# Performance work log

Hardware: AMD Instinct MI355X
Metric: run time of the kernel (lower is better)

The kernel has to match this reference:

```python
import jax, jax.numpy as jnp
import numpy as np

N, E, IN, H, OUT = 50000, 600000, 256, 128, 40
EPS, GAMMA = 0.1, 0.1  # PyG AntiSymmetricConv defaults


def _build_norm(edge_index, n):
    # GCNConv normalization with added self loops: D^-1/2 (A+I) D^-1/2
    loops = jnp.arange(n, dtype=edge_index.dtype)
    src = jnp.concatenate([edge_index[0], loops])
    dst = jnp.concatenate([edge_index[1], loops])
    deg = jax.ops.segment_sum(jnp.ones(src.shape[0], dtype=jnp.float32), dst, num_segments=n)
    dinv = jnp.where(deg > 0, jax.lax.rsqrt(jnp.maximum(deg, 1e-12)), 0.0)
    return src, dst, dinv[src] * dinv[dst]


def _gcn(x, w, src, dst, norm, n):
    # GCNConv(bias=False): scatter normalized messages to target nodes
    m = (x @ w)[src] * norm[:, None]          # [E+N, d]
    return jax.ops.segment_sum(m, dst, num_segments=n)


def _antisym_conv(x, W, gcn_w, bias, src, dst, norm, num_iters):
    d = W.shape[0]
    aW = W - W.T - GAMMA * jnp.eye(d, dtype=W.dtype)  # antisymmetric weight
    n = x.shape[0]

    def step(h, _):
        upd = jnp.tanh(h @ aW.T + _gcn(h, gcn_w, src, dst, norm, n) + bias)
        return h + EPS * upd, None

    x, _ = jax.lax.scan(step, x, None, length=num_iters)
    return x


def setup_inputs() -> dict:
    key = jax.random.key(0)
    ks = jax.random.split(key, 16)
    s = lambda fan: 1.0 / np.sqrt(fan)
    return {
        "x": jax.random.normal(ks[0], (N, IN), dtype=jnp.float32),
        "edge_index": jax.random.randint(ks[1], (2, E), 0, N, dtype=jnp.int64),
        "w_hid": jax.random.normal(ks[2], (H, IN), dtype=jnp.float32) * s(IN),
        "b_hid": jax.random.normal(ks[3], (H,), dtype=jnp.float32) * s(IN),
        "W_a1": jax.random.normal(ks[4], (H, H), dtype=jnp.float32) * s(H),
        "gcn_w1": jax.random.normal(ks[5], (H, H), dtype=jnp.float32) * s(H),
        "b_a1": jax.random.normal(ks[6], (H,), dtype=jnp.float32) * s(H),
        "w_hid2": jax.random.normal(ks[7], (H // 2, H), dtype=jnp.float32) * s(H),
        "b_hid2": jax.random.normal(ks[8], (H // 2,), dtype=jnp.float32) * s(H),
        "W_a2": jax.random.normal(ks[9], (H // 2, H // 2), dtype=jnp.float32) * s(H // 2),
        "gcn_w2": jax.random.normal(ks[10], (H // 2, H // 2), dtype=jnp.float32) * s(H // 2),
        "b_a2": jax.random.normal(ks[11], (H // 2,), dtype=jnp.float32) * s(H // 2),
        "w_fc": jax.random.normal(ks[12], (OUT, H // 2), dtype=jnp.float32) * s(H // 2),
        "b_fc": jax.random.normal(ks[13], (OUT,), dtype=jnp.float32) * s(H // 2),
    }


def reference(x, edge_index, w_hid, b_hid, W_a1, gcn_w1, b_a1,
              w_hid2, b_hid2, W_a2, gcn_w2, b_a2, w_fc, b_fc):
    n = x.shape[0]
    src, dst, norm = _build_norm(edge_index, n)
    h = jax.nn.leaky_relu(x @ w_hid.T + b_hid)          # dropout is no-op in eval
    h = _antisym_conv(h, W_a1, gcn_w1, b_a1, src, dst, norm, num_iters=3)
    h = jax.nn.leaky_relu(h)
    h = jax.nn.leaky_relu(h @ w_hid2.T + b_hid2)
    h = _antisym_conv(h, W_a2, gcn_w2, b_a2, src, dst, norm, num_iters=1)
    out = h @ w_fc.T + b_fc
    return jax.nn.log_softmax(out, axis=1)
```

## Files before the change

kernel.cpp:

```cpp
#include <hip/hip_runtime.h>
#include <hip/hip_bf16.h>
#include <math.h>

typedef unsigned short u16;
typedef unsigned int   u32;
using short8  = __attribute__((ext_vector_type(8))) short;
using f32x4   = __attribute__((ext_vector_type(4))) float;

static constexpr int NNODE = 50000;
static constexpr int NEDGE = 600000;
static constexpr float EPSC   = 0.1f;
static constexpr float GAMMAC = 0.1f;

static constexpr int NTILE = (NNODE + 63) / 64;
static constexpr int GH    = 128;
static constexpr int NRNG  = 12500;
static constexpr int NWORD = NRNG / 2;
static constexpr int NPASS = 4;

static constexpr long long O_DINV   = 0;
static constexpr long long O_DEGI   = 50000;
static constexpr long long O_ROWPTR = 100000;
static constexpr long long O_GCUR   = 150004;
static constexpr long long O_ECSR   = 200260;
static constexpr long long O_WHB    = 1400260;
static constexpr long long O_G1TB   = O_WHB  + 16384;
static constexpr long long O_AW1B   = O_G1TB + 8192;
static constexpr long long O_W2B    = O_AW1B + 8192;
static constexpr long long O_AW2B   = O_W2B  + 4096;
static constexpr long long O_G2TB   = O_AW2B + 2048;
static constexpr long long O_WFCB   = O_G2TB + 2048;
static constexpr long long O_AGGB   = 3450004;
static constexpr long long O_HB0    = O_AGGB + 3200000;
static constexpr long long O_HB1    = O_HB0  + 3200000;
static constexpr long long O_S0     = O_HB1  + 3200000;
static constexpr long long O_S1     = O_S0   + 1600000;
static constexpr long long O_PART   = O_S1   + 1600000;
static constexpr long long O_BASE   = O_PART + 3200000;

__device__ __forceinline__ float bf2f(u16 u) {
    return __uint_as_float(((unsigned)u) << 16);
}
__device__ __forceinline__ u16 f2bf(float f) {
    unsigned u = __float_as_uint(f);
    return (u16)((u + 0x7FFFu + ((u >> 16) & 1u)) >> 16);
}
__device__ __forceinline__ float ftanh(float x) {
    float x2 = fminf(fmaxf(2.f * x, -30.f), 30.f);
    float e = __expf(x2);
    return (e - 1.f) * __builtin_amdgcn_rcpf(e + 1.f);
}
__device__ __forceinline__ u16 pk_fp8(float a, float b) {
    int pk = __builtin_amdgcn_cvt_pk_fp8_f32(a, b, 0, false);
    return (u16)(pk & 0xffff);
}
__device__ __forceinline__ void acc_fp8x4(float* a, u32 v, float w) {
    a[0] += __builtin_amdgcn_cvt_f32_fp8(v, 0) * w;
    a[1] += __builtin_amdgcn_cvt_f32_fp8(v, 1) * w;
    a[2] += __builtin_amdgcn_cvt_f32_fp8(v, 2) * w;
    a[3] += __builtin_amdgcn_cvt_f32_fp8(v, 3) * w;
}

__global__ __launch_bounds__(256) void prep_kernel(
    const float* __restrict__ w_hid, const float* __restrict__ W_a1,
    const float* __restrict__ gcn1,  const float* __restrict__ w2,
    const float* __restrict__ W_a2,  const float* __restrict__ gcn2,
    const float* __restrict__ wfc,   float* __restrict__ ws)
{
    int j = blockIdx.x * 256 + threadIdx.x;
    if (j < 32768) { ((u16*)(ws+O_WHB))[j] = f2bf(w_hid[j]); return; } j -= 32768;
    if (j < 16384) { int r=j>>7, c=j&127; ((u16*)(ws+O_G1TB))[j] = f2bf(gcn1[c*128+r]); return; } j -= 16384;
    if (j < 16384) { int r=j>>7, c=j&127;
                     ((u16*)(ws+O_AW1B))[j] = f2bf(W_a1[r*128+c] - W_a1[c*128+r] - (r==c?GAMMAC:0.f));
                     return; } j -= 16384;
    if (j < 8192)  { ((u16*)(ws+O_W2B))[j] = f2bf(w2[j]); return; } j -= 8192;
    if (j < 4096)  { int r=j>>6, c=j&63;
                     ((u16*)(ws+O_AW2B))[j] = f2bf(W_a2[r*64+c] - W_a2[c*64+r] - (r==c?GAMMAC:0.f));
                     return; } j -= 4096;
    if (j < 4096)  { int r=j>>6, c=j&63; ((u16*)(ws+O_G2TB))[j] = f2bf(gcn2[c*64+r]); return; } j -= 4096;
    if (j < 2560)  { ((u16*)(ws+O_WFCB))[j] = f2bf(wfc[j]); return; } j -= 2560;
    if (j == 0)    { ((int*)(ws+O_GCUR))[0] = 0; }
}

__global__ __launch_bounds__(256) void alloc_kernel(
    const u16* __restrict__ part, float* __restrict__ dinv,
    int* __restrict__ degi, int* __restrict__ rowptr,
    u16* __restrict__ base16, int* __restrict__ gcur)
{
    int i = blockIdx.x * 256 + threadIdx.x;
    int lane = threadIdx.x & 63;
    bool ok = i < NNODE;
    int deg = 0;
    if (ok) {
        int run = 0;
        #pragma unroll 4
        for (int g = 0; g < GH; ++g) {
            base16[(long long)g * NNODE + i] = (u16)run;
            run += part[(long long)g * NNODE + i];
        }
        deg = run;
        degi[i] = deg;
        dinv[i] = rsqrtf(1.0f + (float)deg);
    }
    int run = deg;
    #pragma unroll
    for (int off = 1; off < 64; off <<= 1) {
        int v = __shfl_up(run, off);
        if (lane >= off) run += v;
    }
    int tot = __shfl(run, 63);
    int basep = 0;
    if (lane == 63) basep = atomicAdd(gcur, tot);
    basep = __shfl(basep, 63);
    if (ok) rowptr[i] = basep + run - deg;
}

__global__ __launch_bounds__(256) void fill_kernel(
    const int* __restrict__ ei, const float* __restrict__ dinv,
    const int* __restrict__ rowptr, const u16* __restrict__ base16,
    int2* __restrict__ ecsr)
{
    __shared__ u32 cur[NWORD];
    const int g    = blockIdx.x >> 2;
    const int pass = blockIdx.x & 3;
    const long long e0 = (long long)g * NEDGE / GH;
    const long long e1 = (long long)(g + 1) * NEDGE / GH;
    const u16* bb = base16 + (long long)g * NNODE;
    const int nbase = pass * NRNG;
    for (int wi = threadIdx.x; wi < NWORD; wi += 256) cur[wi] = 0;
    __syncthreads();
    for (long long e = e0 + threadIdx.x; e < e1; e += 256) {
        int d = ei[NEDGE + e];
        int r = d - nbase;
        if ((unsigned)r < (unsigned)NRNG) {
            int s = ei[e];
            u32 old = atomicAdd(&cur[r >> 1], 1u << ((r & 1) * 16));
            int rank = (int)((old >> ((r & 1) * 16)) & 0xffffu);
            int slot = rowptr[d] + (int)bb[d] + rank;
            int2 v;
            v.x = s;
            v.y = __float_as_int(dinv[s]);
            ecsr[slot] = v;
        }
    }
}

template<int KS, int NT, int AF32, int LOADACT, int EPI>
__global__ __launch_bounds__(256, 4) void mgemm(
    const void* __restrict__ Araw,
    const u16* __restrict__ Bt,
    const float* __restrict__ bias,
    float* __restrict__ outF,
    u16* __restrict__ outB,
    u16* __restrict__ outB8,
    int M, int Nn, int ldc,
    const int* __restrict__ ei,
    u16* __restrict__ partial)
{
    constexpr int K    = KS * 32;
    constexpr int KCHU = (K > 128) ? 128 : K;
    constexpr int KC   = KCHU / 32;
    constexpr int NCH  = K / KCHU;
    constexpr int P    = KCHU + 8;
    constexpr int ROWS = NT * 16;
    constexpr int CW   = NT * 16 + 1;
    constexpr int BSZ  = ROWS * P * 2;
    constexpr int ASZ  = 64 * CW * 4;
    constexpr int SMEM = BSZ > ASZ ? BSZ : ASZ;
    __shared__ __align__(16) char smem[SMEM];

    if (ei && blockIdx.x >= NTILE) {
        int g = blockIdx.x - NTILE;
        u32* hist = (u32*)smem;
        const long long e0 = (long long)g * NEDGE / GH;
        const long long e1 = (long long)(g + 1) * NEDGE / GH;
        u16* part = partial + (long long)g * NNODE;
        for (int pass = 0; pass < NPASS; ++pass) {
            const int nbase = pass * NRNG;
            for (int wi = threadIdx.x; wi < NWORD; wi += 256) hist[wi] = 0;
            __syncthreads();
            for (long long e = e0 + threadIdx.x; e < e1; e += 256) {
                int d = ei[NEDGE + e];
                int r = d - nbase;
                if ((unsigned)r < (unsigned)NRNG)
                    atomicAdd(&hist[r >> 1], 1u << ((r & 1) * 16));
            }
            __syncthreads();
            for (int wi = threadIdx.x; wi < NWORD; wi += 256)
                *(u32*)&part[nbase + wi * 2] = hist[wi];
            __syncthreads();
        }
        return;
    }

    u16*   bl   = (u16*)smem;
    float* accL = (float*)smem;

    const int wave = threadIdx.x >> 6;
    const int lane = threadIdx.x & 63;
    const int m = lane & 15, q = lane >> 4;
    const int rowbase = blockIdx.x * 64 + wave * 16;
    const int row = rowbase + m;
    const bool rok = row < M;
    const short8 z8 = {0,0,0,0,0,0,0,0};

    short8 af[KS];
    if (AF32) {
        const float* apf = (const float*)Araw + (long long)row * K;
        #pragma unroll
        for (int k = 0; k < KS; ++k) {
            short8 t = z8;
            if (rok) {
                const float4* p = (const float4*)(apf + (k * 4 + q) * 8);
                float4 a = p[0], b = p[1];
                t[0]=(short)f2bf(a.x); t[1]=(short)f2bf(a.y); t[2]=(short)f2bf(a.z); t[3]=(short)f2bf(a.w);
                t[4]=(short)f2bf(b.x); t[5]=(short)f2bf(b.y); t[6]=(short)f2bf(b.z); t[7]=(short)f2bf(b.w);
            }
            af[k] = t;
        }
    } else {
        const short8* ap = (const short8*)((const u16*)Araw + (long long)row * K);
        #pragma unroll
        for (int k = 0; k < KS; ++k) af[k] = rok ? ap[k * 4 + q] : z8;
    }
    if (LOADACT) {
        #pragma unroll
        for (int k = 0; k < KS; ++k)
            #pragma unroll
            for (int e = 0; e < 8; ++e) {
                float f = bf2f((u16)af[k][e]);
                f = f > 0.f ? f : 0.01f * f;
                af[k][e] = (short)f2bf(f);
            }
    }

    f32x4 acc[NT];
    #pragma unroll
    for (int j = 0; j < NT; ++j) acc[j] = (f32x4){0.f,0.f,0.f,0.f};

    for (int ch = 0; ch < NCH; ++ch) {
        if (ch) __syncthreads();
        constexpr int CHUNKS = ROWS * (KCHU / 8);
        for (int t = threadIdx.x; t < CHUNKS; t += 256) {
            int r = t / (KCHU / 8), c = t - r * (KCHU / 8);
            short8 v = z8;
            if (r < Nn) v = *(const short8*)&Bt[(long long)r * K + ch * KCHU + c * 8];
            *(short8*)&bl[r * P + c * 8] = v;
        }
        __syncthreads();
        #pragma unroll
        for (int j = 0; j < NT; ++j) {
            #pragma unroll
            for (int k = 0; k < KC; ++k) {
                short8 bf_ = *(const short8*)&bl[(j * 16 + m) * P + k * 32 + q * 8];
                acc[j] = __builtin_amdgcn_mfma_f32_16x16x32_bf16(af[ch * KC + k], bf_, acc[j], 0, 0, 0);
            }
        }
    }

    __syncthreads();
    #pragma unroll
    for (int j = 0; j < NT; ++j)
        #pragma unroll
        for (int r = 0; r < 4; ++r)
            accL[(wave * 16 + q * 4 + r) * CW + j * 16 + m] = acc[j][r];
    __syncthreads();

    const int c0 = lane * 2;
    if (c0 < NT * 16) {
        float2 bv = {0.f, 0.f};
        if (bias) {
            if (c0 < Nn)     bv.x = bias[c0];
            if (c0 + 1 < Nn) bv.y = bias[c0 + 1];
        }
        #pragma unroll
        for (int rl = 0; rl < 16; ++rl) {
            int rowD = rowbase + rl;
            if (rowD >= M) continue;
            float2 v = *(const float2*)&accL[(wave * 16 + rl) * CW + c0];
            long long o = (long long)rowD * ldc + c0;
            v.x += bv.x; v.y += bv.y;
            if (EPI == 1) {
                v.x = v.x > 0.f ? v.x : 0.01f * v.x;
                v.y = v.y > 0.f ? v.y : 0.01f * v.y;
            }
            if (c0 + 1 < Nn) {
                if (outB) { ushort2 ob; ob.x = f2bf(v.x); ob.y = f2bf(v.y);
                            *(ushort2*)&outB[o] = ob; }
                if (outB8) outB8[o >> 1] = pk_fp8(v.x, v.y);
                if (outF) { *(float2*)&outF[o] = v; }
            } else if (c0 < Nn) {
                if (outB) outB[o] = f2bf(v.x);
                if (outF) outF[o] = v.x;
            }
        }
    }
}

template<int HD>
__global__ __launch_bounds__(256) void gather_kernel(
    const int* __restrict__ rowptr, const int* __restrict__ degi,
    const int2* __restrict__ ecsr, const float* __restrict__ dinv,
    const u32* __restrict__ g8, u16* __restrict__ aggB)
{
    int node = (blockIdx.x * 256 + threadIdx.x) >> 6;
    int lane = threadIdx.x & 63;
    if (node >= NNODE) return;
    const int qr = lane >> 4, l4 = lane & 15;
    const int r0 = rowptr[node];
    const int r1 = r0 + degi[node];
    const float dn = dinv[node];
    constexpr int EL = (HD == 128) ? 8 : 4;

    float a[EL];
    #pragma unroll
    for (int i = 0; i < EL; ++i) a[i] = 0.f;
    if (qr == 0) {
        if (HD == 128) {
            uint2 gv = ((const uint2*)g8)[(long long)node * 16 + l4];
            acc_fp8x4(a, gv.x, dn);
            acc_fp8x4(a + 4, gv.y, dn);
        } else {
            u32 gv = g8[(long long)node * 16 + l4];
            acc_fp8x4(a, gv, dn);
        }
    }

    for (int base = r0; base < r1; base += 64) {
        int idx = base + lane;
        int cs = 0; float cw = 0.f;
        if (idx < r1) { int2 ev = ecsr[idx]; cs = ev.x; cw = __int_as_float(ev.y); }
        int cnt = min(64, r1 - base);
        for (int j = 0; j < cnt; j += 16) {
            #pragma unroll
            for (int u = 0; u < 4; ++u) {
                int jj = j + u * 4 + qr;
                int   s = __shfl(cs, jj);
                float w = __shfl(cw, jj);
                if (HD == 128) {
                    uint2 gv = ((const uint2*)g8)[(long long)s * 16 + l4];
                    acc_fp8x4(a, gv.x, w);
                    acc_fp8x4(a + 4, gv.y, w);
                } else {
                    u32 gv = g8[(long long)s * 16 + l4];
                    acc_fp8x4(a, gv, w);
                }
            }
        }
    }

    #pragma unroll
    for (int i = 0; i < EL; ++i) {
        a[i] += __shfl_xor(a[i], 16);
        a[i] += __shfl_xor(a[i], 32);
    }
    if (HD == 128) {
        float v0 = (qr == 0) ? a[0] : (qr == 1) ? a[2] : (qr == 2) ? a[4] : a[6];
        float v1 = (qr == 0) ? a[1] : (qr == 1) ? a[3] : (qr == 2) ? a[5] : a[7];
        v0 *= dn; v1 *= dn;
        long long o = (long long)node * 128 + l4 * 8 + qr * 2;
        ushort2 ob; ob.x = f2bf(v0); ob.y = f2bf(v1);
        *(ushort2*)&aggB[o] = ob;
    } else {
        float v = (qr == 0) ? a[0] : (qr == 1) ? a[1] : (qr == 2) ? a[2] : a[3];
        aggB[(long long)node * 64 + l4 * 4 + qr] = f2bf(v * dn);
    }
}

__global__ __launch_bounds__(512, 3) void fconv(
    const u16* __restrict__ hA, const u32* __restrict__ g8,
    const int* __restrict__ rowptr, const int* __restrict__ degi,
    const int2* __restrict__ ecsr, const float* __restrict__ dinv,
    const u16* __restrict__ BtW, const u16* __restrict__ BtG,
    const float* __restrict__ bias,
    u16* __restrict__ outB, u16* __restrict__ outB8)
{
    constexpr int K = 128, P = 136;
    __shared__ __align__(16) char smem[52224];
    u16* bl   = (u16*)smem;
    u16* aggT = (u16*)(smem + 34816);
    const int wave = threadIdx.x >> 6, lane = threadIdx.x & 63;
    const int m = lane & 15, q = lane >> 4;
    const int blockrow = blockIdx.x * 64;
    const short8 z8 = {0,0,0,0,0,0,0,0};

    {
        const int qr = q, l4 = m;
        for (int nn = 0; nn < 8; ++nn) {
            int lr = wave * 8 + nn;
            int node = blockrow + lr;
            if (node >= NNODE) break;
            const int r0 = rowptr[node];
            const int r1 = r0 + degi[node];
            const float dn = dinv[node];
            float a[8] = {0.f,0.f,0.f,0.f,0.f,0.f,0.f,0.f};
            if (qr == 0) {
                uint2 gv = ((const uint2*)g8)[(long long)node * 16 + l4];
                acc_fp8x4(a, gv.x, dn);
                acc_fp8x4(a + 4, gv.y, dn);
            }
            for (int base = r0; base < r1; base += 64) {
                int idx = base + lane;
                int cs = 0; float cw = 0.f;
                if (idx < r1) { int2 ev = ecsr[idx]; cs = ev.x; cw = __int_as_float(ev.y); }
                int cnt = min(64, r1 - base);
                for (int j = 0; j < cnt; j += 16) {
                    #pragma unroll
                    for (int u = 0; u < 4; ++u) {
                        int jj = j + u * 4 + qr;
                        int   s = __shfl(cs, jj);
                        float w = __shfl(cw, jj);
                        uint2 gv = ((const uint2*)g8)[(long long)s * 16 + l4];
                        acc_fp8x4(a, gv.x, w);
                        acc_fp8x4(a + 4, gv.y, w);
                    }
                }
            }
            #pragma unroll
            for (int i = 0; i < 8; ++i) {
                a[i] += __shfl_xor(a[i], 16);
                a[i] += __shfl_xor(a[i], 32);
            }
            float v0 = (qr == 0) ? a[0] : (qr == 1) ? a[2] : (qr == 2) ? a[4] : a[6];
            float v1 = (qr == 0) ? a[1] : (qr == 1) ? a[3] : (qr == 2) ? a[5] : a[7];
            v0 *= dn; v1 *= dn;
            ushort2 ob; ob.x = f2bf(v0); ob.y = f2bf(v1);
            *(ushort2*)&aggT[lr * P + l4 * 8 + qr * 2] = ob;
        }
    }
    __syncthreads();

    const int nh = wave >> 2;
    const int rowbase = blockrow + (wave & 3) * 16;
    const int row = rowbase + m;
    const bool rok = row < NNODE;

    short8 af1[4], af2[4];
    {
        const short8* ap1 = (const short8*)(hA + (long long)row * K);
        #pragma unroll
        for (int k = 0; k < 4; ++k) {
            af1[k] = rok ? ap1[k * 4 + q] : z8;
            af2[k] = rok ? *(const short8*)&aggT[((wave & 3) * 16 + m) * P + k * 32 + q * 8] : z8;
        }
    }

    f32x4 acc[4];
    #pragma unroll
    for (int j = 0; j < 4; ++j) acc[j] = (f32x4){0.f,0.f,0.f,0.f};

    #pragma unroll
    for (int pass = 0; pass < 2; ++pass) {
        const u16* Bsrc = pass ? BtG : BtW;
        if (pass) __syncthreads();
        for (int t = threadIdx.x; t < 2048; t += 512) {
            int r = t >> 4, c = t & 15;
            *(short8*)&bl[r * P + c * 8] = *(const short8*)&Bsrc[(long long)r * K + c * 8];
        }
        __syncthreads();
        #pragma unroll
        for (int j = 0; j < 4; ++j)
            #pragma unroll
            for (int kk = 0; kk < 4; ++kk) {
                short8 b_ = *(const short8*)&bl[(nh*64 + j*16 + m) * P + kk*32 + q*8];
                acc[j] = __builtin_amdgcn_mfma_f32_16x16x32_bf16(
                    pass ? af2[kk] : af1[kk], b_, acc[j], 0, 0, 0);
            }
    }

    __syncthreads();
    float* accW = (float*)smem + wave * 16 * 65;
    #pragma unroll
    for (int j = 0; j < 4; ++j)
        #pragma unroll
        for (int r = 0; r < 4; ++r)
            accW[(q*4 + r) * 65 + j*16 + m] = acc[j][r];

    const int hw = lane >> 5;
    const int c0 = (lane & 31) * 2;
    float2 bv = {bias[nh*64 + c0], bias[nh*64 + c0 + 1]};
    #pragma unroll
    for (int rl8 = 0; rl8 < 8; ++rl8) {
        int rl = hw * 8 + rl8;
        int rowD = rowbase + rl;
        if (rowD >= NNODE) continue;
        float2 v = *(const float2*)&accW[rl * 65 + c0];
        long long o = (long long)rowD * 128 + nh*64 + c0;
        ushort2 hh = *(const ushort2*)&hA[o];
        float n0 = bf2f(hh.x) + EPSC * ftanh(v.x + bv.x);
        float n1 = bf2f(hh.y) + EPSC * ftanh(v.y + bv.y);
        ushort2 ob; ob.x = f2bf(n0); ob.y = f2bf(n1);
        *(ushort2*)&outB[o] = ob;
        outB8[o >> 1] = pk_fp8(n0, n1);
    }
}

template<int KS, int NT, int TAIL>
__global__ __launch_bounds__(256, 4) void mgemm_conv(
    const u16* __restrict__ hA,
    const u16* __restrict__ gA,
    const u16* __restrict__ BtW,
    const u16* __restrict__ BtG,
    const float* __restrict__ bias,
    u16* __restrict__ outB,
    u16* __restrict__ outB8,
    const u16* __restrict__ w2W,
    const float* __restrict__ b2,
    int M)
{
    constexpr int K    = KS * 32;
    constexpr int Nn   = NT * 16;
    constexpr int P    = K + 8;
    constexpr int CW   = Nn + 1;
    constexpr int BSZ  = Nn * P * 2;
    constexpr int ASZ  = 64 * CW * 4;
    constexpr int R1   = BSZ > ASZ ? BSZ : ASZ;
    __shared__ __align__(16) char smem[R1];
    u16*   bl   = (u16*)smem;
    float* accL = (float*)smem;

    const int wave = threadIdx.x >> 6;
    const int lane = threadIdx.x & 63;
    const int m = lane & 15, q = lane >> 4;
    const int rowbase = blockIdx.x * 64 + wave * 16;
    const int row = rowbase + m;
    const bool rok = row < M;
    const short8 z8 = {0,0,0,0,0,0,0,0};

    short8 af1[KS], af2[KS];
    {
        const short8* ap1 = (const short8*)(hA + (long long)row * K);
        const short8* ap2 = (const short8*)(gA + (long long)row * K);
        #pragma unroll
        for (int k = 0; k < KS; ++k) {
            af1[k] = rok ? ap1[k * 4 + q] : z8;
            af2[k] = rok ? ap2[k * 4 + q] : z8;
        }
    }

    f32x4 acc[NT];
    #pragma unroll
    for (int j = 0; j < NT; ++j) acc[j] = (f32x4){0.f,0.f,0.f,0.f};

    #pragma unroll
    for (int pass = 0; pass < 2; ++pass) {
        const u16* Bcur = pass ? BtG : BtW;
        if (pass) __syncthreads();
        constexpr int CHUNKS = Nn * (K / 8);
        for (int t = threadIdx.x; t < CHUNKS; t += 256) {
            int r = t / (K / 8), c = t - r * (K / 8);
            *(short8*)&bl[r * P + c * 8] = *(const short8*)&Bcur[(long long)r * K + c * 8];
        }
        __syncthreads();
        #pragma unroll
        for (int j = 0; j < NT; ++j) {
            #pragma unroll
            for (int k = 0; k < KS; ++k) {
                short8 bf_ = *(const short8*)&bl[(j * 16 + m) * P + k * 32 + q * 8];
                acc[j] = __builtin_amdgcn_mfma_f32_16x16x32_bf16(
                    pass ? af2[k] : af1[k], bf_, acc[j], 0, 0, 0);
            }
        }
    }

    __syncthreads();
    #pragma unroll
    for (int j = 0; j < NT; ++j)
        #pragma unroll
        for (int r = 0; r < 4; ++r)
            accL[(wave * 16 + q * 4 + r) * CW + j * 16 + m] = acc[j][r];
    __syncthreads();

    const int c0 = lane * 2;
    if (TAIL == 0) {
        if (c0 < Nn) {
            float2 bv = {bias[c0], bias[c0 + 1]};
            #pragma unroll
            for (int rl = 0; rl < 16; ++rl) {
                int rowD = rowbase + rl;
                if (rowD >= M) continue;
                float2 v = *(const float2*)&accL[(wave * 16 + rl) * CW + c0];
                long long o = (long long)rowD * Nn + c0;
                ushort2 hh = *(const ushort2*)&hA[o];
                float n0 = bf2f(hh.x) + EPSC * ftanh(v.x + bv.x);
                float n1 = bf2f(hh.y) + EPSC * ftanh(v.y + bv.y);
                ushort2 ob; ob.x = f2bf(n0); ob.y = f2bf(n1);
                *(ushort2*)&outB[o] = ob;
                if (outB8) outB8[o >> 1] = pk_fp8(n0, n1);
            }
        }
        return;
    }

    u32 hv[16];
    {
        float2 bv = {bias[c0], bias[c0 + 1]};
        #pragma unroll
        for (int rl = 0; rl < 16; ++rl) {
            int rowD = rowbase + rl;
            float n0 = 0.f, n1 = 0.f;
            if (rowD < M) {
                float2 v = *(const float2*)&accL[(wave * 16 + rl) * CW + c0];
                long long o = (long long)rowD * K + c0;
                ushort2 hh = *(const ushort2*)&hA[o];
                n0 = bf2f(hh.x) + EPSC * ftanh(v.x + bv.x);
                n1 = bf2f(hh.y) + EPSC * ftanh(v.y + bv.y);
                n0 = n0 > 0.f ? n0 : 0.01f * n0;
                n1 = n1 > 0.f ? n1 : 0.01f * n1;
            }
            hv[rl] = (u32)f2bf(n0) | ((u32)f2bf(n1) << 16);
        }
    }
    __syncthreads();

    u16* aggT = (u16*)smem;
    u16* bl2  = (u16*)(smem + 17408);
    #pragma unroll
    for (int rl = 0; rl < 16; ++rl)
        *(u32*)&aggT[(wave * 16 + rl) * P + c0] = hv[rl];
    for (int t = threadIdx.x; t < 1024; t += 256) {
        int r = t >> 4, c = t & 15;
        *(short8*)&bl2[r * P + c * 8] = *(const short8*)&w2W[(long long)r * K + c * 8];
    }
    __syncthreads();

    short8 af3[4];
    #pragma unroll
    for (int k = 0; k < 4; ++k)
        af3[k] = *(const short8*)&aggT[(wave * 16 + m) * P + k * 32 + q * 8];

    f32x4 acc2[4];
    #pragma unroll
    for (int j = 0; j < 4; ++j) acc2[j] = (f32x4){0.f,0.f,0.f,0.f};
    #pragma unroll
    for (int j = 0; j < 4; ++j)
        #pragma unroll
        for (int k = 0; k < 4; ++k) {
            short8 bf_ = *(const short8*)&bl2[(j * 16 + m) * P + k * 32 + q * 8];
            acc2[j] = __builtin_amdgcn_mfma_f32_16x16x32_bf16(af3[k], bf_, acc2[j], 0, 0, 0);
        }

    __syncthreads();
    constexpr int CW2 = 65;
    float* accL2 = (float*)smem;
    #pragma unroll
    for (int j = 0; j < 4; ++j)
        #pragma unroll
        for (int r = 0; r < 4; ++r)
            accL2[(wave * 16 + q * 4 + r) * CW2 + j * 16 + m] = acc2[j][r];
    __syncthreads();

    if (c0 < 64) {
        float2 bv = {b2[c0], b2[c0 + 1]};
        #pragma unroll
        for (int rl = 0; rl < 16; ++rl) {
            int rowD = rowbase + rl;
            if (rowD >= M) continue;
            float2 v = *(const float2*)&accL2[(wave * 16 + rl) * CW2 + c0];
            v.x += bv.x; v.y += bv.y;
            v.x = v.x > 0.f ? v.x : 0.01f * v.x;
            v.y = v.y > 0.f ? v.y : 0.01f * v.y;
            long long o = (long long)rowD * 64 + c0;
            ushort2 ob; ob.x = f2bf(v.x); ob.y = f2bf(v.y);
            *(ushort2*)&outB[o] = ob;
            outB8[o >> 1] = pk_fp8(v.x, v.y);
        }
    }
}

__global__ __launch_bounds__(256, 4) void conv2fc(
    const u16* __restrict__ hA,
    const u16* __restrict__ gA,
    const u16* __restrict__ BtW, const u16* __restrict__ BtG,
    const float* __restrict__ bias,
    const u16* __restrict__ wfcB, const float* __restrict__ bfc,
    float* __restrict__ outF, int M)
{
    constexpr int K  = 64, NT = 4, KS = 2;
    constexpr int P  = K + 8;
    constexpr int CW = 65;
    constexpr int R1 = 64 * CW * 4;
    __shared__ __align__(16) char smem[R1 + 64 * P * 2];
    u16*   bl   = (u16*)smem;
    float* accL = (float*)smem;
    u16*   aggT = (u16*)(smem + R1);

    const int wave = threadIdx.x >> 6;
    const int lane = threadIdx.x & 63;
    const int m = lane & 15, q = lane >> 4;
    const int rowbase = blockIdx.x * 64 + wave * 16;
    const int row = rowbase + m;
    const bool rok = row < M;
    const short8 z8 = {0,0,0,0,0,0,0,0};

    short8 af1[KS], af2[KS];
    {
        const short8* ap1 = (const short8*)(hA + (long long)row * K);
        const short8* ap2 = (const short8*)(gA + (long long)row * K);
        #pragma unroll
        for (int k = 0; k < KS; ++k) {
            af1[k] = rok ? ap1[k * 4 + q] : z8;
            af2[k] = rok ? ap2[k * 4 + q] : z8;
        }
    }

    f32x4 acc[NT];
    #pragma unroll
    for (int j = 0; j < NT; ++j) acc[j] = (f32x4){0.f,0.f,0.f,0.f};

    #pragma unroll
    for (int pass = 0; pass < 2; ++pass) {
        const u16* Bcur = pass ? BtG : BtW;
        if (pass) __syncthreads();
        constexpr int CHUNKS = 64 * (K / 8);
        for (int t = threadIdx.x; t < CHUNKS; t += 256) {
            int r = t >> 3, c = t & 7;
            *(short8*)&bl[r * P + c * 8] = *(const short8*)&Bcur[(long long)r * K + c * 8];
        }
        __syncthreads();
        #pragma unroll
        for (int j = 0; j < NT; ++j)
            #pragma unroll
            for (int k = 0; k < KS; ++k) {
                short8 bf_ = *(const short8*)&bl[(j * 16 + m) * P + k * 32 + q * 8];
                acc[j] = __builtin_amdgcn_mfma_f32_16x16x32_bf16(
                    pass ? af2[k] : af1[k], bf_, acc[j], 0, 0, 0);
            }
    }

    __syncthreads();
    #pragma unroll
    for (int j = 0; j < NT; ++j)
        #pragma unroll
        for (int r = 0; r < 4; ++r)
            accL[(wave * 16 + q * 4 + r) * CW + j * 16 + m] = acc[j][r];
    __syncthreads();

    {
        const int c0 = lane * 2;
        float2 bv = {bias[c0 & 63], bias[(c0 + 1) & 63]};
        if (c0 < 64) {
            #pragma unroll
            for (int rl = 0; rl < 16; ++rl) {
                int rowD = rowbase + rl;
                float n0 = 0.f, n1 = 0.f;
                if (rowD < M) {
                    float2 v = *(const float2*)&accL[(wave * 16 + rl) * CW + c0];
                    long long o = (long long)rowD * 64 + c0;
                    ushort2 hh = *(const ushort2*)&hA[o];
                    n0 = bf2f(hh.x) + EPSC * ftanh(v.x + bv.x);
                    n1 = bf2f(hh.y) + EPSC * ftanh(v.y + bv.y);
                }
                ushort2 ob; ob.x = f2bf(n0); ob.y = f2bf(n1);
                *(ushort2*)&aggT[(wave * 16 + rl) * P + c0] = ob;
            }
        }
    }
    __syncthreads();

    short8 af4[KS];
    #pragma unroll
    for (int k = 0; k < KS; ++k)
        af4[k] = *(const short8*)&aggT[(wave * 16 + m) * P + k * 32 + q * 8];

    {
        constexpr int CHF = 48 * 8;
        for (int t = threadIdx.x; t < CHF; t += 256) {
            int r = t >> 3, c = t & 7;
            short8 v = z8;
            if (r < 40) v = *(const short8*)&wfcB[(long long)r * K + c * 8];
            *(short8*)&bl[r * P + c * 8] = v;
        }
    }
    __syncthreads();

    f32x4 acc3[3];
    #pragma unroll
    for (int j = 0; j < 3; ++j) acc3[j] = (f32x4){0.f,0.f,0.f,0.f};
    #pragma unroll
    for (int j = 0; j < 3; ++j)
        #pragma unroll
        for (int k = 0; k < KS; ++k) {
            short8 bf_ = *(const short8*)&bl[(j * 16 + m) * P + k * 32 + q * 8];
            acc3[j] = __builtin_amdgcn_mfma_f32_16x16x32_bf16(af4[k], bf_, acc3[j], 0, 0, 0);
        }

    __syncthreads();
    constexpr int CW3 = 49;
    #pragma unroll
    for (int j = 0; j < 3; ++j)
        #pragma unroll
        for (int r = 0; r < 4; ++r)
            accL[(wave * 16 + q * 4 + r) * CW3 + j * 16 + m] = acc3[j][r];
    __syncthreads();

    float mrow = 0.f, lrow = 0.f;
    if (lane < 16) {
        const float* rp = &accL[(wave * 16 + lane) * CW3];
        float mx = -1e30f;
        for (int c = 0; c < 40; ++c) mx = fmaxf(mx, rp[c] + bfc[c]);
        float s = 0.f;
        for (int c = 0; c < 40; ++c) s += expf(rp[c] + bfc[c] - mx);
        mrow = mx; lrow = logf(s);
    }
    for (int rl = 0; rl < 16; ++rl) {
        float mm = __shfl(mrow, rl);
        float ll = __shfl(lrow, rl);
        int rowD = rowbase + rl;
        if (rowD < M && lane < 40) {
            float v = accL[(wave * 16 + rl) * CW3 + lane] + bfc[lane];
            outF[(long long)rowD * 40 + lane] = v - mm - ll;
        }
    }
}

extern "C" void kernel_launch(void* const* d_in, const int* in_sizes, int n_in,
                              void* d_out, int out_size, void* d_ws, size_t ws_size,
                              hipStream_t stream) {
    const float* x     = (const float*)d_in[0];
    const int*   ei    = (const int*)d_in[1];
    const float* w_hid = (const float*)d_in[2];
    const float* b_hid = (const float*)d_in[3];
    const float* W_a1  = (const float*)d_in[4];
    const float* gcn1  = (const float*)d_in[5];
    const float* b_a1  = (const float*)d_in[6];
    const float* w2    = (const float*)d_in[7];
    const float* b2    = (const float*)d_in[8];
    const float* W_a2  = (const float*)d_in[9];
    const float* gcn2  = (const float*)d_in[10];
    const float* b_a2  = (const float*)d_in[11];
    const float* wfc   = (const float*)d_in[12];
    const float* bfc   = (const float*)d_in[13];
    float* ws = (float*)d_ws;
    float* out = (float*)d_out;

    float* dinv   = ws + O_DINV;
    int*   degi   = (int*)(ws + O_DEGI);
    int*   rowptr = (int*)(ws + O_ROWPTR);
    int*   gcur   = (int*)(ws + O_GCUR);
    int2*  ecsr   = (int2*)(ws + O_ECSR);
    u16* whB  = (u16*)(ws + O_WHB);
    u16* g1tB = (u16*)(ws + O_G1TB);
    u16* aw1B = (u16*)(ws + O_AW1B);
    u16* w2B  = (u16*)(ws + O_W2B);
    u16* aw2B = (u16*)(ws + O_AW2B);
    u16* g2tB = (u16*)(ws + O_G2TB);
    u16* wfcB = (u16*)(ws + O_WFCB);
    u16* aggB = (u16*)(ws + O_AGGB);
    u16* hB0  = (u16*)(ws + O_HB0);
    u16* hB1  = (u16*)(ws + O_HB1);
    u16* s0   = (u16*)(ws + O_S0);
    u16* s1   = (u16*)(ws + O_S1);
    u16* part = (u16*)(ws + O_PART);
    u16* base16 = (u16*)(ws + O_BASE);

    prep_kernel<<<(84481 + 255) / 256, 256, 0, stream>>>(
        w_hid, W_a1, gcn1, w2, W_a2, gcn2, wfc, ws);

    const int gatherBlocks = (NNODE * 64 + 255) / 256;

    mgemm<8, 8, 1, 0, 1><<<NTILE + GH, 256, 0, stream>>>(
        x, whB, b_hid, nullptr, hB0, s0, NNODE, 128, 128, ei, part);

    alloc_kernel<<<(NNODE + 255) / 256, 256, 0, stream>>>(
        part, dinv, degi, rowptr, base16, gcur);
    fill_kernel<<<GH * NPASS, 256, 0, stream>>>(ei, dinv, rowptr, base16, ecsr);

    fconv<<<NTILE, 512, 0, stream>>>(hB0, (const u32*)s0, rowptr, degi, ecsr, dinv,
                                     aw1B, g1tB, b_a1, hB1, s1);
    gather_kernel<128><<<gatherBlocks, 256, 0, stream>>>(
        rowptr, degi, ecsr, dinv, (const u32*)s1, aggB);
    mgemm_conv<4, 8, 0><<<NTILE, 256, 0, stream>>>(
        hB1, aggB, aw1B, g1tB, b_a1, hB0, s0, nullptr, nullptr, NNODE);
    gather_kernel<128><<<gatherBlocks, 256, 0, stream>>>(
        rowptr, degi, ecsr, dinv, (const u32*)s0, aggB);
    mgemm_conv<4, 8, 1><<<NTILE, 256, 0, stream>>>(
        hB0, aggB, aw1B, g1tB, b_a1, hB1, s1, w2B, b2, NNODE);

    gather_kernel<64><<<gatherBlocks, 256, 0, stream>>>(
        rowptr, degi, ecsr, dinv, (const u32*)s1, aggB);
    conv2fc<<<NTILE, 256, 0, stream>>>(
        hB1, aggB, aw2B, g2tB, b_a2, wfcB, bfc, out, NNODE);
}
```

Measured before the change: 355.9 us.

## Use fused gather-GEMM fconv kernel for all three conv iterations, including hidden2 tail

The separate gather_kernel plus mgemm_conv launches for conv iterations two and three are replaced by the fused fconv kernel, which aggregates neighbors into shared memory and runs the GEMM in one launch. A TAIL variant adds the leaky-ReLU, hidden2 linear layer and bias epilogue inside fconv. This removes the global round trip of the aggregated buffer and two kernel launches. In exchange fconv carries more shared-memory and register pressure and an extra synchronized GEMM phase.

```diff
diff --git a/kernel.cpp b/kernel.cpp
--- a/kernel.cpp
+++ b/kernel.cpp
@@ -367,13 +367,15 @@
     }
 }
 
+template<int TAIL>
 __global__ __launch_bounds__(512, 3) void fconv(
     const u16* __restrict__ hA, const u32* __restrict__ g8,
     const int* __restrict__ rowptr, const int* __restrict__ degi,
     const int2* __restrict__ ecsr, const float* __restrict__ dinv,
     const u16* __restrict__ BtW, const u16* __restrict__ BtG,
     const float* __restrict__ bias,
-    u16* __restrict__ outB, u16* __restrict__ outB8)
+    u16* __restrict__ outB, u16* __restrict__ outB8,
+    const u16* __restrict__ w2W, const float* __restrict__ b2)
 {
     constexpr int K = 128, P = 136;
     __shared__ __align__(16) char smem[52224];
@@ -479,192 +481,90 @@
     const int hw = lane >> 5;
     const int c0 = (lane & 31) * 2;
     float2 bv = {bias[nh*64 + c0], bias[nh*64 + c0 + 1]};
+
+    if (TAIL == 0) {
+        #pragma unroll
+        for (int rl8 = 0; rl8 < 8; ++rl8) {
+            int rl = hw * 8 + rl8;
+            int rowD = rowbase + rl;
+            if (rowD >= NNODE) continue;
+            float2 v = *(const float2*)&accW[rl * 65 + c0];
+            long long o = (long long)rowD * 128 + nh*64 + c0;
+            ushort2 hh = *(const ushort2*)&hA[o];
+            float n0 = bf2f(hh.x) + EPSC * ftanh(v.x + bv.x);
+            float n1 = bf2f(hh.y) + EPSC * ftanh(v.y + bv.y);
+            ushort2 ob; ob.x = f2bf(n0); ob.y = f2bf(n1);
+            *(ushort2*)&outB[o] = ob;
+            outB8[o >> 1] = pk_fp8(n0, n1);
+        }
+        return;
+    }
+
     #pragma unroll
     for (int rl8 = 0; rl8 < 8; ++rl8) {
         int rl = hw * 8 + rl8;
         int rowD = rowbase + rl;
+        float n0 = 0.f, n1 = 0.f;
+        if (rowD < NNODE) {
+            float2 v = *(const float2*)&accW[rl * 65 + c0];
+            long long o = (long long)rowD * 128 + nh*64 + c0;
+            ushort2 hh = *(const ushort2*)&hA[o];
+            n0 = bf2f(hh.x) + EPSC * ftanh(v.x + bv.x);
+            n1 = bf2f(hh.y) + EPSC * ftanh(v.y + bv.y);
+            n0 = n0 > 0.f ? n0 : 0.01f * n0;
+            n1 = n1 > 0.f ? n1 : 0.01f * n1;
+        }
+        ushort2 ob; ob.x = f2bf(n0); ob.y = f2bf(n1);
+        *(ushort2*)&aggT[((wave & 3) * 16 + rl) * P + nh*64 + c0] = ob;
+    }
+    __syncthreads();
+
+    short8 af3[4];
+    #pragma unroll
+    for (int k = 0; k < 4; ++k)
+        af3[k] = *(const short8*)&aggT[((wave & 3) * 16 + m) * P + k * 32 + q * 8];
+
+    for (int t = threadIdx.x; t < 1024; t += 512) {
+        int r = t >> 4, c = t & 15;
+        *(short8*)&bl[r * P + c * 8] = *(const short8*)&w2W[(long long)r * K + c * 8];
+    }
+    __syncthreads();
+
+    f32x4 acc2[2];
+    #pragma unroll
+    for (int j = 0; j < 2; ++j) acc2[j] = (f32x4){0.f,0.f,0.f,0.f};
+    #pragma unroll
+    for (int j = 0; j < 2; ++j)
+        #pragma unroll
+        for (int k = 0; k < 4; ++k) {
+            short8 b_ = *(const short8*)&bl[(nh*32 + j*16 + m) * P + k*32 + q*8];
+            acc2[j] = __builtin_amdgcn_mfma_f32_16x16x32_bf16(af3[k], b_, acc2[j], 0, 0, 0);
+        }
+
+    __syncthreads();
+    float* accW2 = (float*)smem + wave * 16 * 33;
+    #pragma unroll
+    for (int j = 0; j < 2; ++j)
+        #pragma unroll
+        for (int r = 0; r < 4; ++r)
+            accW2[(q*4 + r) * 33 + j*16 + m] = acc2[j][r];
+
+    const int r4 = lane >> 4;
+    const int c2 = (lane & 15) * 2;
+    float2 bv2 = {b2[nh*32 + c2], b2[nh*32 + c2 + 1]};
+    #pragma unroll
+    for (int rr = 0; rr < 4; ++rr) {
+        int rl = r4 * 4 + rr;
+        int rowD = rowbase + rl;
         if (rowD >= NNODE) continue;
-        float2 v = *(const float2*)&accW[rl * 65 + c0];
-        long long o = (long long)rowD * 128 + nh*64 + c0;
-        ushort2 hh = *(const ushort2*)&hA[o];
-        float n0 = bf2f(hh.x) + EPSC * ftanh(v.x + bv.x);
-        float n1 = bf2f(hh.y) + EPSC * ftanh(v.y + bv.y);
-        ushort2 ob; ob.x = f2bf(n0); ob.y = f2bf(n1);
+        float2 v = *(const float2*)&accW2[rl * 33 + c2];
+        v.x += bv2.x; v.y += bv2.y;
+        v.x = v.x > 0.f ? v.x : 0.01f * v.x;
+        v.y = v.y > 0.f ? v.y : 0.01f * v.y;
+        long long o = (long long)rowD * 64 + nh*32 + c2;
+        ushort2 ob; ob.x = f2bf(v.x); ob.y = f2bf(v.y);
         *(ushort2*)&outB[o] = ob;
-        outB8[o >> 1] = pk_fp8(n0, n1);
-    }
-}
-
-template<int KS, int NT, int TAIL>
-__global__ __launch_bounds__(256, 4) void mgemm_conv(
-    const u16* __restrict__ hA,
-    const u16* __restrict__ gA,
-    const u16* __restrict__ BtW,
-    const u16* __restrict__ BtG,
-    const float* __restrict__ bias,
-    u16* __restrict__ outB,
-    u16* __restrict__ outB8,
-    const u16* __restrict__ w2W,
-    const float* __restrict__ b2,
-    int M)
-{
-    constexpr int K    = KS * 32;
-    constexpr int Nn   = NT * 16;
-    constexpr int P    = K + 8;
-    constexpr int CW   = Nn + 1;
-    constexpr int BSZ  = Nn * P * 2;
-    constexpr int ASZ  = 64 * CW * 4;
-    constexpr int R1   = BSZ > ASZ ? BSZ : ASZ;
-    __shared__ __align__(16) char smem[R1];
-    u16*   bl   = (u16*)smem;
-    float* accL = (float*)smem;
-
-    const int wave = threadIdx.x >> 6;
-    const int lane = threadIdx.x & 63;
-    const int m = lane & 15, q = lane >> 4;
-    const int rowbase = blockIdx.x * 64 + wave * 16;
-    const int row = rowbase + m;
-    const bool rok = row < M;
-    const short8 z8 = {0,0,0,0,0,0,0,0};
-
-    short8 af1[KS], af2[KS];
-    {
-        const short8* ap1 = (const short8*)(hA + (long long)row * K);
-        const short8* ap2 = (const short8*)(gA + (long long)row * K);
-        #pragma unroll
-        for (int k = 0; k < KS; ++k) {
-            af1[k] = rok ? ap1[k * 4 + q] : z8;
-            af2[k] = rok ? ap2[k * 4 + q] : z8;
-        }
-    }
-
-    f32x4 acc[NT];
-    #pragma unroll
-    for (int j = 0; j < NT; ++j) acc[j] = (f32x4){0.f,0.f,0.f,0.f};
-
-    #pragma unroll
-    for (int pass = 0; pass < 2; ++pass) {
-        const u16* Bcur = pass ? BtG : BtW;
-        if (pass) __syncthreads();
-        constexpr int CHUNKS = Nn * (K / 8);
-        for (int t = threadIdx.x; t < CHUNKS; t += 256) {
-            int r = t / (K / 8), c = t - r * (K / 8);
-            *(short8*)&bl[r * P + c * 8] = *(const short8*)&Bcur[(long long)r * K + c * 8];
-        }
-        __syncthreads();
-        #pragma unroll
-        for (int j = 0; j < NT; ++j) {
-            #pragma unroll
-            for (int k = 0; k < KS; ++k) {
-                short8 bf_ = *(const short8*)&bl[(j * 16 + m) * P + k * 32 + q * 8];
-                acc[j] = __builtin_amdgcn_mfma_f32_16x16x32_bf16(
-                    pass ? af2[k] : af1[k], bf_, acc[j], 0, 0, 0);
-            }
-        }
-    }
-
-    __syncthreads();
-    #pragma unroll
-    for (int j = 0; j < NT; ++j)
-        #pragma unroll
-        for (int r = 0; r < 4; ++r)
-            accL[(wave * 16 + q * 4 + r) * CW + j * 16 + m] = acc[j][r];
-    __syncthreads();
-
-    const int c0 = lane * 2;
-    if (TAIL == 0) {
-        if (c0 < Nn) {
-            float2 bv = {bias[c0], bias[c0 + 1]};
-            #pragma unroll
-            for (int rl = 0; rl < 16; ++rl) {
-                int rowD = rowbase + rl;
-                if (rowD >= M) continue;
-                float2 v = *(const float2*)&accL[(wave * 16 + rl) * CW + c0];
-                long long o = (long long)rowD * Nn + c0;
-                ushort2 hh = *(const ushort2*)&hA[o];
-                float n0 = bf2f(hh.x) + EPSC * ftanh(v.x + bv.x);
-                float n1 = bf2f(hh.y) + EPSC * ftanh(v.y + bv.y);
-                ushort2 ob; ob.x = f2bf(n0); ob.y = f2bf(n1);
-                *(ushort2*)&outB[o] = ob;
-                if (outB8) outB8[o >> 1] = pk_fp8(n0, n1);
-            }
-        }
-        return;
-    }
-
-    u32 hv[16];
-    {
-        float2 bv = {bias[c0], bias[c0 + 1]};
-        #pragma unroll
-        for (int rl = 0; rl < 16; ++rl) {
-            int rowD = rowbase + rl;
-            float n0 = 0.f, n1 = 0.f;
-            if (rowD < M) {
-                float2 v = *(const float2*)&accL[(wave * 16 + rl) * CW + c0];
-                long long o = (long long)rowD * K + c0;
-                ushort2 hh = *(const ushort2*)&hA[o];
-                n0 = bf2f(hh.x) + EPSC * ftanh(v.x + bv.x);
-                n1 = bf2f(hh.y) + EPSC * ftanh(v.y + bv.y);
-                n0 = n0 > 0.f ? n0 : 0.01f * n0;
-                n1 = n1 > 0.f ? n1 : 0.01f * n1;
-            }
-            hv[rl] = (u32)f2bf(n0) | ((u32)f2bf(n1) << 16);
-        }
-    }
-    __syncthreads();
-
-    u16* aggT = (u16*)smem;
-    u16* bl2  = (u16*)(smem + 17408);
-    #pragma unroll
-    for (int rl = 0; rl < 16; ++rl)
-        *(u32*)&aggT[(wave * 16 + rl) * P + c0] = hv[rl];
-    for (int t = threadIdx.x; t < 1024; t += 256) {
-        int r = t >> 4, c = t & 15;
-        *(short8*)&bl2[r * P + c * 8] = *(const short8*)&w2W[(long long)r * K + c * 8];
-    }
-    __syncthreads();
-
-    short8 af3[4];
-    #pragma unroll
-    for (int k = 0; k < 4; ++k)
-        af3[k] = *(const short8*)&aggT[(wave * 16 + m) * P + k * 32 + q * 8];
-
-    f32x4 acc2[4];
-    #pragma unroll
-    for (int j = 0; j < 4; ++j) acc2[j] = (f32x4){0.f,0.f,0.f,0.f};
-    #pragma unroll
-    for (int j = 0; j < 4; ++j)
-        #pragma unroll
-        for (int k = 0; k < 4; ++k) {
-            short8 bf_ = *(const short8*)&bl2[(j * 16 + m) * P + k * 32 + q * 8];
-            acc2[j] = __builtin_amdgcn_mfma_f32_16x16x32_bf16(af3[k], bf_, acc2[j], 0, 0, 0);
-        }
-
-    __syncthreads();
-    constexpr int CW2 = 65;
-    float* accL2 = (float*)smem;
-    #pragma unroll
-    for (int j = 0; j < 4; ++j)
-        #pragma unroll
-        for (int r = 0; r < 4; ++r)
-            accL2[(wave * 16 + q * 4 + r) * CW2 + j * 16 + m] = acc2[j][r];
-    __syncthreads();
-
-    if (c0 < 64) {
-        float2 bv = {b2[c0], b2[c0 + 1]};
-        #pragma unroll
-        for (int rl = 0; rl < 16; ++rl) {
-            int rowD = rowbase + rl;
-            if (rowD >= M) continue;
-            float2 v = *(const float2*)&accL2[(wave * 16 + rl) * CW2 + c0];
-            v.x += bv.x; v.y += bv.y;
-            v.x = v.x > 0.f ? v.x : 0.01f * v.x;
-            v.y = v.y > 0.f ? v.y : 0.01f * v.y;
-            long long o = (long long)rowD * 64 + c0;
-            ushort2 ob; ob.x = f2bf(v.x); ob.y = f2bf(v.y);
-            *(ushort2*)&outB[o] = ob;
-            outB8[o >> 1] = pk_fp8(v.x, v.y);
-        }
+        outB8[o >> 1] = pk_fp8(v.x, v.y);
     }
 }
 
@@ -866,16 +766,12 @@
         part, dinv, degi, rowptr, base16, gcur);
     fill_kernel<<<GH * NPASS, 256, 0, stream>>>(ei, dinv, rowptr, base16, ecsr);
 
-    fconv<<<NTILE, 512, 0, stream>>>(hB0, (const u32*)s0, rowptr, degi, ecsr, dinv,
-                                     aw1B, g1tB, b_a1, hB1, s1);
-    gather_kernel<128><<<gatherBlocks, 256, 0, stream>>>(
-        rowptr, degi, ecsr, dinv, (const u32*)s1, aggB);
-    mgemm_conv<4, 8, 0><<<NTILE, 256, 0, stream>>>(
-        hB1, aggB, aw1B, g1tB, b_a1, hB0, s0, nullptr, nullptr, NNODE);
-    gather_kernel<128><<<gatherBlocks, 256, 0, stream>>>(
-        rowptr, degi, ecsr, dinv, (const u32*)s0, aggB);
-    mgemm_conv<4, 8, 1><<<NTILE, 256, 0, stream>>>(
-        hB0, aggB, aw1B, g1tB, b_a1, hB1, s1, w2B, b2, NNODE);
+    fconv<0><<<NTILE, 512, 0, stream>>>(hB0, (const u32*)s0, rowptr, degi, ecsr, dinv,
+                                        aw1B, g1tB, b_a1, hB1, s1, nullptr, nullptr);
+    fconv<0><<<NTILE, 512, 0, stream>>>(hB1, (const u32*)s1, rowptr, degi, ecsr, dinv,
+                                        aw1B, g1tB, b_a1, hB0, s0, nullptr, nullptr);
+    fconv<1><<<NTILE, 512, 0, stream>>>(hB0, (const u32*)s0, rowptr, degi, ecsr, dinv,
+                                        aw1B, g1tB, b_a1, hB1, s1, w2B, b2);
 
     gather_kernel<64><<<gatherBlocks, 256, 0, stream>>>(
         rowptr, degi, ecsr, dinv, (const u32*)s1, aggB);
```

New measurement: 355.9 us, median of 2. No clear change (+0.0%).
